# Kernel optimization log

Hardware: AMD Instinct MI355X
Metric: run time of the kernel (lower is better)

## Reference

```python
import jax, jax.numpy as jnp
import numpy as np

EPS = 1e-5
B, T, IN, EMD, CELL, OUT = 32768, 128, 2, 128, 128, 5


def batchnorm(x, gamma, beta):
    # BatchNorm1d in training mode: biased batch stats over batch dim
    mu = jnp.mean(x, axis=0, keepdims=True)
    var = jnp.var(x, axis=0, keepdims=True)
    return gamma * (x - mu) * jax.lax.rsqrt(var + EPS) + beta


def setup_inputs() -> dict:
    key = jax.random.key(0)
    ks = jax.random.split(key, 8)
    s = 0.05
    return {
        "inputs": jax.random.normal(ks[0], (B, T, IN), dtype=jnp.float32),
        # input embedding MLP: Linear(2,128) + BN + ReLU
        "w_emb": jax.random.normal(ks[1], (EMD, IN), dtype=jnp.float32) * s,
        "b_emb": jnp.zeros((EMD,), dtype=jnp.float32),
        "gamma1": jnp.ones((EMD,), dtype=jnp.float32),
        "beta1": jnp.zeros((EMD,), dtype=jnp.float32),
        # LSTMCell(emd_size, cell_size): gate order i,f,g,o
        "w_ih": jax.random.normal(ks[2], (4 * CELL, EMD), dtype=jnp.float32) * s,
        "w_hh": jax.random.normal(ks[3], (4 * CELL, CELL), dtype=jnp.float32) * s,
        "b_ih": jnp.zeros((4 * CELL,), dtype=jnp.float32),
        "b_hh": jnp.zeros((4 * CELL,), dtype=jnp.float32),
        # output MLP: Linear(128,5) + BN + ReLU
        "w_out": jax.random.normal(ks[4], (OUT, CELL), dtype=jnp.float32) * s,
        "b_out": jnp.zeros((OUT,), dtype=jnp.float32),
        "gamma2": jnp.ones((OUT,), dtype=jnp.float32),
        "beta2": jnp.zeros((OUT,), dtype=jnp.float32),
    }


def reference(inputs, w_emb, b_emb, gamma1, beta1, w_ih, w_hh, b_ih, b_hh,
              w_out, b_out, gamma2, beta2):
    x_tbd = jnp.transpose(inputs, (1, 0, 2))  # [T, B, IN]

    def step(carry, x_t):
        h, c = carry
        # input embedding MLP (train-mode BN + ReLU)
        e = jax.nn.relu(batchnorm(x_t @ w_emb.T + b_emb, gamma1, beta1))
        # LSTM cell
        gates = e @ w_ih.T + b_ih + h @ w_hh.T + b_hh  # [B, 4*CELL]
        i, f, g, o = jnp.split(gates, 4, axis=-1)
        c_new = jax.nn.sigmoid(f) * c + jax.nn.sigmoid(i) * jnp.tanh(g)
        h_new = jax.nn.sigmoid(o) * jnp.tanh(c_new)
        # output MLP (train-mode BN + ReLU)
        y = jax.nn.relu(batchnorm(h_new @ w_out.T + b_out, gamma2, beta2))
        return (h_new, c_new), y

    h0 = jnp.zeros((inputs.shape[0], CELL), dtype=inputs.dtype)
    c0 = jnp.zeros((inputs.shape[0], CELL), dtype=inputs.dtype)
    _, ys = jax.lax.scan(step, (h0, c0), x_tbd)  # ys: [T, B, OUT]
    return jnp.transpose(ys, (1, 0, 2))  # [B, T, OUT]
```

## Files before the change

### kernel.cpp

```cpp
#include <hip/hip_runtime.h>
#include <math.h>

#define B_    32768
#define T_    128
#define OUT_  5
#define EPS_  1e-5f

typedef float f32x4 __attribute__((ext_vector_type(4)));
typedef __bf16 bfrag __attribute__((ext_vector_type(8)));
typedef unsigned short ushort_t;

#define WS_WC2   0
#define WS_GB    67584
#define WS_A0    68112
#define WS_A1    84496
#define WS_C     100880
#define WS_IST   117264
#define WS_ZST   117904

__device__ __forceinline__ ushort_t f2bf(float f) {
  unsigned u = __float_as_uint(f);
  u += 0x7FFFu + ((u >> 16) & 1u);
  return (ushort_t)(u >> 16);
}
__device__ __forceinline__ float fsig(float x) {
  return __builtin_amdgcn_rcpf(1.f + __expf(-x));
}
__device__ __forceinline__ float ftanh(float x) {
  return 1.f - 2.f * __builtin_amdgcn_rcpf(1.f + __expf(2.f * x));
}

__global__ void k_istats(const float* __restrict__ x, float* __restrict__ istats) {
  const int tid = threadIdx.x;
  const int t = tid >> 1;
  const int i = tid & 1;
  const long b0 = (long)blockIdx.x * 64;
  float s_v = 0.f, s_vv = 0.f, s_cross = 0.f;
  for (int s = 0; s < 64; ++s) {
    float v = x[(b0 + s) * 256 + tid];
    float p = __shfl_xor(v, 1);
    s_v += v; s_vv += v * v; s_cross += v * p;
  }
  float* st = istats + t * 5;
  if (i == 0) {
    atomicAdd(st + 0, s_v); atomicAdd(st + 2, s_vv); atomicAdd(st + 4, s_cross);
  } else {
    atomicAdd(st + 1, s_v); atomicAdd(st + 3, s_vv);
  }
}

__global__ void k_prep_w(const float* __restrict__ w_ih, const float* __restrict__ w_hh,
                         const float* __restrict__ w_out, const float* __restrict__ b_ih,
                         const float* __restrict__ b_hh, const float* __restrict__ b_out,
                         ushort_t* __restrict__ Wc2, float* __restrict__ gbias) {
  int idx = blockIdx.x * 256 + threadIdx.x;
  int e = idx & 7;
  int lm = (idx >> 3) & 15;
  int lq = (idx >> 7) & 3;
  int ks = (idx >> 9) & 7;
  int T = idx >> 12;
  int k = ks * 32 + lq * 8 + e;
  float v;
  if (T < 32) {
    int g = T * 16 + lm;
    v = (k < 128) ? w_ih[g * 128 + k] : w_hh[g * 128 + (k - 128)];
  } else {
    v = (k >= 128 && lm < OUT_) ? w_out[lm * 128 + (k - 128)] : 0.f;
  }
  Wc2[idx] = f2bf(v);
  if (idx < 528) {
    float bv = (idx < 512) ? b_ih[idx] + b_hh[idx]
                           : (idx < 517 ? b_out[idx - 512] : 0.f);
    gbias[idx] = bv;
  }
}

__global__ void k_coef(const float* __restrict__ istats, const float* __restrict__ w_emb,
                       const float* __restrict__ b_emb, const float* __restrict__ gamma1,
                       const float* __restrict__ beta1, float* __restrict__ A0,
                       float* __restrict__ A1, float* __restrict__ C) {
  int idx = blockIdx.x * 256 + threadIdx.x;
  int t = idx >> 7, f = idx & 127;
  const float* st = istats + t * 5;
  const float invB = 1.f / (float)B_;
  float m0 = st[0] * invB, m1 = st[1] * invB;
  float v00 = st[2] * invB - m0 * m0;
  float v11 = st[3] * invB - m1 * m1;
  float c01 = st[4] * invB - m0 * m1;
  float w0 = w_emb[f * 2 + 0], w1 = w_emb[f * 2 + 1];
  float mu = m0 * w0 + m1 * w1 + b_emb[f];
  float var = w0 * w0 * v00 + w1 * w1 * v11 + 2.f * w0 * w1 * c01;
  float alpha = gamma1[f] * rsqrtf(var + EPS_);
  A0[t * 128 + f] = alpha * w0;
  A1[t * 128 + f] = alpha * w1;
  C[t * 128 + f] = alpha * (b_emb[f] - mu) + beta1[f];
}

__global__ __launch_bounds__(512, 2) void k_lstm(
    const float* __restrict__ x, const ushort_t* __restrict__ Wc2,
    const float* __restrict__ gbias, const float* __restrict__ A0,
    const float* __restrict__ A1, const float* __restrict__ Cc,
    float* __restrict__ out, float* __restrict__ zstats) {
  __shared__ __align__(16) ushort_t Abuf[128][520];
  __shared__ float zredS[2][8][5], zredQ[2][8][5];

  const int tid = threadIdx.x;
  const int w = tid >> 6;
  const int l = tid & 63;
  const int lm = l & 15;
  const int lq = l >> 4;
  const long b0 = (long)blockIdx.x * 128;

  const uint4* W4 = (const uint4*)Wc2;

  uint4 wreg[4][8];
#pragma unroll
  for (int i = 0; i < 4; ++i)
#pragma unroll
    for (int ks = 0; ks < 8; ++ks)
      wreg[i][ks] = W4[((w + 8 * i) * 8 + ks) * 64 + l];
  uint4 wzr[4];
#pragma unroll
  for (int i = 0; i < 4; ++i) wzr[i] = W4[(32 * 8 + 4 + i) * 64 + l];

  float bias_g[4];
#pragma unroll
  for (int i = 0; i < 4; ++i) bias_g[i] = gbias[(w + 8 * i) * 16 + lm];
  const float bias_z = gbias[512 + lm];

  const int em = (w << 4) + (l >> 2);
  const int ec = l & 3;
  const float2* x2 = (const float2*)x;

  float cst[8][4];
#pragma unroll
  for (int mt = 0; mt < 8; ++mt)
#pragma unroll
    for (int r = 0; r < 4; ++r) cst[mt][r] = 0.f;

  f32x4 zh0 = {0.f, 0.f, 0.f, 0.f}, zh1 = zh0, zh2 = zh0, zh3 = zh0;

  for (int i = tid; i < 128 * 520 / 8; i += 512)
    ((uint4*)&Abuf[0][0])[i] = make_uint4(0u, 0u, 0u, 0u);
  __syncthreads();

  for (int t = 0; t <= T_; ++t) {
    const int p = t & 1;
    const int pe = p * 128;
    const int ph = 256 + (p ^ 1) * 128;
    const int hw = 256 + p * 128;

    if (t < T_) {
      float2 xv = x2[(size_t)(b0 + em) * 128 + t];
#pragma unroll
      for (int pp = 0; pp < 4; ++pp) {
        const int f0 = pp * 32 + ec * 8;
        const f32x4 a0l = *(const f32x4*)(A0 + t * 128 + f0);
        const f32x4 a0h = *(const f32x4*)(A0 + t * 128 + f0 + 4);
        const f32x4 a1l = *(const f32x4*)(A1 + t * 128 + f0);
        const f32x4 a1h = *(const f32x4*)(A1 + t * 128 + f0 + 4);
        const f32x4 ccl = *(const f32x4*)(Cc + t * 128 + f0);
        const f32x4 cch = *(const f32x4*)(Cc + t * 128 + f0 + 4);
        unsigned pk[4];
#pragma unroll
        for (int h2 = 0; h2 < 4; ++h2) {
          float e0, e1;
          if (h2 < 2) {
            e0 = fmaf(xv.x, a0l[h2 * 2], fmaf(xv.y, a1l[h2 * 2], ccl[h2 * 2]));
            e1 = fmaf(xv.x, a0l[h2 * 2 + 1], fmaf(xv.y, a1l[h2 * 2 + 1], ccl[h2 * 2 + 1]));
          } else {
            e0 = fmaf(xv.x, a0h[(h2 - 2) * 2], fmaf(xv.y, a1h[(h2 - 2) * 2], cch[(h2 - 2) * 2]));
            e1 = fmaf(xv.x, a0h[(h2 - 2) * 2 + 1],
                      fmaf(xv.y, a1h[(h2 - 2) * 2 + 1], cch[(h2 - 2) * 2 + 1]));
          }
          e0 = fmaxf(e0, 0.f); e1 = fmaxf(e1, 0.f);
          pk[h2] = (unsigned)f2bf(e0) | ((unsigned)f2bf(e1) << 16);
        }
        *(uint4*)&Abuf[em][pe + f0] = make_uint4(pk[0], pk[1], pk[2], pk[3]);
      }
    }
    __syncthreads();

    if (t >= 2 && tid < 10) {
      const int o = tid >> 1, kind = tid & 1;
      float s = 0.f;
#pragma unroll
      for (int ww = 0; ww < 8; ++ww)
        s += kind ? zredQ[p ^ 1][ww][o] : zredS[p ^ 1][ww][o];
      atomicAdd(&zstats[(size_t)(t - 2) * 10 + o * 2 + kind], s);
    }

    const int colA = lq * 8;

#pragma unroll
    for (int mt = 0; mt < 8; ++mt) {
      const ushort_t* arow = &Abuf[mt * 16 + lm][0];
      f32x4 acc0 = {bias_g[0], bias_g[0], bias_g[0], bias_g[0]};
      f32x4 acc1 = {bias_g[1], bias_g[1], bias_g[1], bias_g[1]};
      f32x4 acc2 = {bias_g[2], bias_g[2], bias_g[2], bias_g[2]};
      f32x4 acc3 = {bias_g[3], bias_g[3], bias_g[3], bias_g[3]};
#pragma unroll
      for (int ks = 0; ks < 8; ++ks) {
        const int col = (ks < 4 ? pe + ks * 32 : ph + (ks - 4) * 32) + colA;
        const bfrag Af = __builtin_bit_cast(bfrag, *(const uint4*)(arow + col));
        acc0 = __builtin_amdgcn_mfma_f32_16x16x32_bf16(
            Af, __builtin_bit_cast(bfrag, wreg[0][ks]), acc0, 0, 0, 0);
        acc1 = __builtin_amdgcn_mfma_f32_16x16x32_bf16(
            Af, __builtin_bit_cast(bfrag, wreg[1][ks]), acc1, 0, 0, 0);
        acc2 = __builtin_amdgcn_mfma_f32_16x16x32_bf16(
            Af, __builtin_bit_cast(bfrag, wreg[2][ks]), acc2, 0, 0, 0);
        acc3 = __builtin_amdgcn_mfma_f32_16x16x32_bf16(
            Af, __builtin_bit_cast(bfrag, wreg[3][ks]), acc3, 0, 0, 0);
      }

      if (mt == w) {
        f32x4 zac = {bias_z, bias_z, bias_z, bias_z};
#pragma unroll
        for (int i = 0; i < 4; ++i) {
          const bfrag Af =
              __builtin_bit_cast(bfrag, *(const uint4*)(arow + ph + i * 32 + colA));
          zac = __builtin_amdgcn_mfma_f32_16x16x32_bf16(
              Af, __builtin_bit_cast(bfrag, wzr[i]), zac, 0, 0, 0);
        }
        if (t > 0) {
          float sz = 0.f, sq = 0.f;
#pragma unroll
          for (int r = 0; r < 4; ++r) {
            const float zv = zac[r];
            sz += zv; sq += zv * zv;
          }
          sz += __shfl_xor(sz, 16); sz += __shfl_xor(sz, 32);
          sq += __shfl_xor(sq, 16); sq += __shfl_xor(sq, 32);
          if (lq == 0 && lm < OUT_) { zredS[p][w][lm] = sz; zredQ[p][w][lm] = sq; }
          const int j = (t - 1) & 3;
          if (j == 0) zh0 = zac;
          else if (j == 1) zh1 = zac;
          else if (j == 2) zh2 = zac;
          else zh3 = zac;
          if (j == 3 && lm < OUT_) {
            const size_t sb0 = (size_t)(b0 + (w << 4) + lq * 4) * (T_ * OUT_) +
                               (size_t)(t - 4) * OUT_ + lm;
#pragma unroll
            for (int r = 0; r < 4; ++r) {
              const size_t sb = sb0 + (size_t)r * (T_ * OUT_);
              out[sb]            = zh0[r];
              out[sb + OUT_]     = zh1[r];
              out[sb + 2 * OUT_] = zh2[r];
              out[sb + 3 * OUT_] = zh3[r];
            }
          }
        }
      }

      if (t < T_) {
#pragma unroll
        for (int r = 0; r < 4; ++r) {
          const float gi = acc0[r], gf = acc1[r], gg = acc2[r], go = acc3[r];
          const float ig = fsig(gi), fg = fsig(gf), g2 = ftanh(gg), og = fsig(go);
          const float cn = fmaf(fg, cst[mt][r], ig * g2);
          cst[mt][r] = cn;
          const float h = og * ftanh(cn);
          Abuf[mt * 16 + lq * 4 + r][hw + (w << 4) + lm] = f2bf(h);
        }
      }
    }
  }

  __syncthreads();
  if (tid < 10) {
    const int o = tid >> 1, kind = tid & 1;
    float s = 0.f;
#pragma unroll
    for (int ww = 0; ww < 8; ++ww) s += kind ? zredQ[0][ww][o] : zredS[0][ww][o];
    atomicAdd(&zstats[(size_t)(T_ - 1) * 10 + o * 2 + kind], s);
  }
}

__global__ void k_outbn(float* __restrict__ out, const float* __restrict__ zstats,
                        const float* __restrict__ gamma2, const float* __restrict__ beta2) {
  int idx = blockIdx.x * 256 + threadIdx.x;
  int r = idx % 640;
  int t = r / 5, o = r - t * 5;
  float z = out[idx];
  float sum = zstats[t * 10 + o * 2];
  float ss = zstats[t * 10 + o * 2 + 1];
  float mu = sum * (1.f / (float)B_);
  float var = ss * (1.f / (float)B_) - mu * mu;
  float y = gamma2[o] * (z - mu) * rsqrtf(var + EPS_) + beta2[o];
  out[idx] = fmaxf(y, 0.f);
}

extern "C" void kernel_launch(void* const* d_in, const int* in_sizes, int n_in, void* d_out,
                              int out_size, void* d_ws, size_t ws_size, hipStream_t stream) {
  const float* x = (const float*)d_in[0];
  const float* w_emb = (const float*)d_in[1];
  const float* b_emb = (const float*)d_in[2];
  const float* gamma1 = (const float*)d_in[3];
  const float* beta1 = (const float*)d_in[4];
  const float* w_ih = (const float*)d_in[5];
  const float* w_hh = (const float*)d_in[6];
  const float* b_ih = (const float*)d_in[7];
  const float* b_hh = (const float*)d_in[8];
  const float* w_out = (const float*)d_in[9];
  const float* b_out = (const float*)d_in[10];
  const float* gamma2 = (const float*)d_in[11];
  const float* beta2 = (const float*)d_in[12];
  float* out = (float*)d_out;
  float* ws = (float*)d_ws;

  ushort_t* Wc2 = (ushort_t*)(ws + WS_WC2);
  float* gbias = ws + WS_GB;
  float* A0 = ws + WS_A0;
  float* A1 = ws + WS_A1;
  float* C = ws + WS_C;
  float* istats = ws + WS_IST;
  float* zstats = ws + WS_ZST;

  hipMemsetAsync(istats, 0, 640 * sizeof(float), stream);
  hipMemsetAsync(zstats, 0, 1280 * sizeof(float), stream);

  k_istats<<<512, 256, 0, stream>>>(x, istats);
  k_prep_w<<<528, 256, 0, stream>>>(w_ih, w_hh, w_out, b_ih, b_hh, b_out, Wc2, gbias);
  k_coef<<<64, 256, 0, stream>>>(istats, w_emb, b_emb, gamma1, beta1, A0, A1, C);
  k_lstm<<<256, 512, 0, stream>>>(x, Wc2, gbias, A0, A1, C, out, zstats);
  k_outbn<<<(B_ * T_ * OUT_) / 256, 256, 0, stream>>>(out, zstats, gamma2, beta2);
}
```

Measured before the change: 1.558 ms.

## Split LDS into swizzled E/H buffers and prefetch next-step embedding before barrier

Replaces the padded shared A buffer with separate double-buffered, XOR-swizzled embedding and hidden-state tiles. The next step's embedding is computed after the MFMA/gate work, so each timestep needs one barrier instead of two, and the extra t==T iteration becomes a peeled epilogue. It also switches to hardware bf16 pack conversion and raises wave priority around the MFMA block. This aims to cut barrier stalls, LDS bank conflicts and conversion ALU cost. The cost is more complex indexing and a separate tail path that must stay consistent with the per-step zstats/output handling.

```diff
diff --git a/kernel.cpp b/kernel.cpp
--- a/kernel.cpp
+++ b/kernel.cpp
@@ -22,6 +22,11 @@
   unsigned u = __float_as_uint(f);
   u += 0x7FFFu + ((u >> 16) & 1u);
   return (ushort_t)(u >> 16);
+}
+__device__ __forceinline__ unsigned cvtpk(float lo, float hi) {
+  unsigned r;
+  asm("v_cvt_pk_bf16_f32 %0, %1, %2" : "=v"(r) : "v"(lo), "v"(hi));
+  return r;
 }
 __device__ __forceinline__ float fsig(float x) {
   return __builtin_amdgcn_rcpf(1.f + __expf(-x));
@@ -96,12 +101,43 @@
   C[t * 128 + f] = alpha * (b_emb[f] - mu) + beta1[f];
 }
 
+__device__ __forceinline__ void stage_e(const float* __restrict__ A0,
+                                        const float* __restrict__ A1,
+                                        const float* __restrict__ Cc, int tt,
+                                        char* erow, float2 xv, const int* ewz, int ec) {
+  const float* A0t = A0 + tt * 128;
+  const float* A1t = A1 + tt * 128;
+  const float* Cct = Cc + tt * 128;
+#pragma unroll
+  for (int pp = 0; pp < 4; ++pp) {
+    const int f0 = pp * 32 + ec * 8;
+    const f32x4 a0l = *(const f32x4*)(A0t + f0);
+    const f32x4 a0h = *(const f32x4*)(A0t + f0 + 4);
+    const f32x4 a1l = *(const f32x4*)(A1t + f0);
+    const f32x4 a1h = *(const f32x4*)(A1t + f0 + 4);
+    const f32x4 ccl = *(const f32x4*)(Cct + f0);
+    const f32x4 cch = *(const f32x4*)(Cct + f0 + 4);
+    unsigned pk[4];
+#pragma unroll
+    for (int j = 0; j < 2; ++j) {
+      float e0 = fmaf(xv.x, a0l[2 * j],     fmaf(xv.y, a1l[2 * j],     ccl[2 * j]));
+      float e1 = fmaf(xv.x, a0l[2 * j + 1], fmaf(xv.y, a1l[2 * j + 1], ccl[2 * j + 1]));
+      pk[j] = cvtpk(fmaxf(e0, 0.f), fmaxf(e1, 0.f));
+      float e2 = fmaf(xv.x, a0h[2 * j],     fmaf(xv.y, a1h[2 * j],     cch[2 * j]));
+      float e3 = fmaf(xv.x, a0h[2 * j + 1], fmaf(xv.y, a1h[2 * j + 1], cch[2 * j + 1]));
+      pk[2 + j] = cvtpk(fmaxf(e2, 0.f), fmaxf(e3, 0.f));
+    }
+    *(uint4*)(erow + ewz[pp]) = make_uint4(pk[0], pk[1], pk[2], pk[3]);
+  }
+}
+
 __global__ __launch_bounds__(512, 2) void k_lstm(
     const float* __restrict__ x, const ushort_t* __restrict__ Wc2,
     const float* __restrict__ gbias, const float* __restrict__ A0,
     const float* __restrict__ A1, const float* __restrict__ Cc,
     float* __restrict__ out, float* __restrict__ zstats) {
-  __shared__ __align__(16) ushort_t Abuf[128][520];
+  __shared__ __align__(16) ushort_t Els[2][128][128];
+  __shared__ __align__(16) ushort_t Hls[2][128][128];
   __shared__ float zredS[2][8][5], zredQ[2][8][5];
 
   const int tid = threadIdx.x;
@@ -132,6 +168,16 @@
   const int ec = l & 3;
   const float2* x2 = (const float2*)x;
 
+  const int rowb = lm * 256;
+  int cswz[4], ewz[4], hoff[4];
+#pragma unroll
+  for (int i = 0; i < 4; ++i) {
+    cswz[i] = (((i * 4 + lq) ^ (lm & 7)) << 4);
+    ewz[i] = (((i * 4 + ec) ^ (em & 7)) << 4);
+    const int rr = lq * 4 + i;
+    hoff[i] = rr * 256 + ((((2 * w) + (lm >> 3)) ^ (rr & 7)) << 4) + ((lm & 7) << 1);
+  }
+
   float cst[8][4];
 #pragma unroll
   for (int mt = 0; mt < 8; ++mt)
@@ -140,46 +186,19 @@
 
   f32x4 zh0 = {0.f, 0.f, 0.f, 0.f}, zh1 = zh0, zh2 = zh0, zh3 = zh0;
 
-  for (int i = tid; i < 128 * 520 / 8; i += 512)
-    ((uint4*)&Abuf[0][0])[i] = make_uint4(0u, 0u, 0u, 0u);
+  for (int i = tid; i < 2048; i += 512)
+    ((uint4*)&Hls[1][0][0])[i] = make_uint4(0u, 0u, 0u, 0u);
+  {
+    float2 xv0 = x2[(size_t)(b0 + em) * 128 + 0];
+    stage_e(A0, A1, Cc, 0, (char*)&Els[0][0][0] + em * 256, xv0, ewz, ec);
+  }
   __syncthreads();
 
-  for (int t = 0; t <= T_; ++t) {
+  for (int t = 0; t < T_; ++t) {
     const int p = t & 1;
-    const int pe = p * 128;
-    const int ph = 256 + (p ^ 1) * 128;
-    const int hw = 256 + p * 128;
-
-    if (t < T_) {
-      float2 xv = x2[(size_t)(b0 + em) * 128 + t];
-#pragma unroll
-      for (int pp = 0; pp < 4; ++pp) {
-        const int f0 = pp * 32 + ec * 8;
-        const f32x4 a0l = *(const f32x4*)(A0 + t * 128 + f0);
-        const f32x4 a0h = *(const f32x4*)(A0 + t * 128 + f0 + 4);
-        const f32x4 a1l = *(const f32x4*)(A1 + t * 128 + f0);
-        const f32x4 a1h = *(const f32x4*)(A1 + t * 128 + f0 + 4);
-        const f32x4 ccl = *(const f32x4*)(Cc + t * 128 + f0);
-        const f32x4 cch = *(const f32x4*)(Cc + t * 128 + f0 + 4);
-        unsigned pk[4];
-#pragma unroll
-        for (int h2 = 0; h2 < 4; ++h2) {
-          float e0, e1;
-          if (h2 < 2) {
-            e0 = fmaf(xv.x, a0l[h2 * 2], fmaf(xv.y, a1l[h2 * 2], ccl[h2 * 2]));
-            e1 = fmaf(xv.x, a0l[h2 * 2 + 1], fmaf(xv.y, a1l[h2 * 2 + 1], ccl[h2 * 2 + 1]));
-          } else {
-            e0 = fmaf(xv.x, a0h[(h2 - 2) * 2], fmaf(xv.y, a1h[(h2 - 2) * 2], cch[(h2 - 2) * 2]));
-            e1 = fmaf(xv.x, a0h[(h2 - 2) * 2 + 1],
-                      fmaf(xv.y, a1h[(h2 - 2) * 2 + 1], cch[(h2 - 2) * 2 + 1]));
-          }
-          e0 = fmaxf(e0, 0.f); e1 = fmaxf(e1, 0.f);
-          pk[h2] = (unsigned)f2bf(e0) | ((unsigned)f2bf(e1) << 16);
-        }
-        *(uint4*)&Abuf[em][pe + f0] = make_uint4(pk[0], pk[1], pk[2], pk[3]);
-      }
-    }
-    __syncthreads();
+
+    float2 xv_nxt = make_float2(0.f, 0.f);
+    if (t + 1 < T_) xv_nxt = x2[(size_t)(b0 + em) * 128 + t + 1];
 
     if (t >= 2 && tid < 10) {
       const int o = tid >> 1, kind = tid & 1;
@@ -190,19 +209,23 @@
       atomicAdd(&zstats[(size_t)(t - 2) * 10 + o * 2 + kind], s);
     }
 
-    const int colA = lq * 8;
+    const char* Ep = (const char*)&Els[p][0][0];
+    const char* Hp1 = (const char*)&Hls[p ^ 1][0][0];
+    char* Hw = (char*)&Hls[p][0][0];
 
 #pragma unroll
     for (int mt = 0; mt < 8; ++mt) {
-      const ushort_t* arow = &Abuf[mt * 16 + lm][0];
+      const int mtoff = mt << 12;
+      const char* eb = Ep + mtoff + rowb;
+      const char* hb = Hp1 + mtoff + rowb;
       f32x4 acc0 = {bias_g[0], bias_g[0], bias_g[0], bias_g[0]};
       f32x4 acc1 = {bias_g[1], bias_g[1], bias_g[1], bias_g[1]};
       f32x4 acc2 = {bias_g[2], bias_g[2], bias_g[2], bias_g[2]};
       f32x4 acc3 = {bias_g[3], bias_g[3], bias_g[3], bias_g[3]};
-#pragma unroll
-      for (int ks = 0; ks < 8; ++ks) {
-        const int col = (ks < 4 ? pe + ks * 32 : ph + (ks - 4) * 32) + colA;
-        const bfrag Af = __builtin_bit_cast(bfrag, *(const uint4*)(arow + col));
+      __builtin_amdgcn_s_setprio(1);
+#pragma unroll
+      for (int ks = 0; ks < 4; ++ks) {
+        const bfrag Af = __builtin_bit_cast(bfrag, *(const uint4*)(eb + cswz[ks]));
         acc0 = __builtin_amdgcn_mfma_f32_16x16x32_bf16(
             Af, __builtin_bit_cast(bfrag, wreg[0][ks]), acc0, 0, 0, 0);
         acc1 = __builtin_amdgcn_mfma_f32_16x16x32_bf16(
@@ -212,47 +235,58 @@
         acc3 = __builtin_amdgcn_mfma_f32_16x16x32_bf16(
             Af, __builtin_bit_cast(bfrag, wreg[3][ks]), acc3, 0, 0, 0);
       }
-
-      if (mt == w) {
+#pragma unroll
+      for (int ks = 0; ks < 4; ++ks) {
+        const bfrag Af = __builtin_bit_cast(bfrag, *(const uint4*)(hb + cswz[ks]));
+        acc0 = __builtin_amdgcn_mfma_f32_16x16x32_bf16(
+            Af, __builtin_bit_cast(bfrag, wreg[0][4 + ks]), acc0, 0, 0, 0);
+        acc1 = __builtin_amdgcn_mfma_f32_16x16x32_bf16(
+            Af, __builtin_bit_cast(bfrag, wreg[1][4 + ks]), acc1, 0, 0, 0);
+        acc2 = __builtin_amdgcn_mfma_f32_16x16x32_bf16(
+            Af, __builtin_bit_cast(bfrag, wreg[2][4 + ks]), acc2, 0, 0, 0);
+        acc3 = __builtin_amdgcn_mfma_f32_16x16x32_bf16(
+            Af, __builtin_bit_cast(bfrag, wreg[3][4 + ks]), acc3, 0, 0, 0);
+      }
+      __builtin_amdgcn_s_setprio(0);
+
+      if (mt == w && t > 0) {
         f32x4 zac = {bias_z, bias_z, bias_z, bias_z};
 #pragma unroll
         for (int i = 0; i < 4; ++i) {
-          const bfrag Af =
-              __builtin_bit_cast(bfrag, *(const uint4*)(arow + ph + i * 32 + colA));
+          const bfrag Af = __builtin_bit_cast(bfrag, *(const uint4*)(hb + cswz[i]));
           zac = __builtin_amdgcn_mfma_f32_16x16x32_bf16(
               Af, __builtin_bit_cast(bfrag, wzr[i]), zac, 0, 0, 0);
         }
-        if (t > 0) {
-          float sz = 0.f, sq = 0.f;
+        float sz = 0.f, sq = 0.f;
+#pragma unroll
+        for (int r = 0; r < 4; ++r) {
+          const float zv = zac[r];
+          sz += zv; sq += zv * zv;
+        }
+        sz += __shfl_xor(sz, 16); sz += __shfl_xor(sz, 32);
+        sq += __shfl_xor(sq, 16); sq += __shfl_xor(sq, 32);
+        if (lq == 0 && lm < OUT_) { zredS[p][w][lm] = sz; zredQ[p][w][lm] = sq; }
+        const int j = (t - 1) & 3;
+        if (j == 0) zh0 = zac;
+        else if (j == 1) zh1 = zac;
+        else if (j == 2) zh2 = zac;
+        else zh3 = zac;
+        if (j == 3 && lm < OUT_) {
+          const size_t sb0 = (size_t)(b0 + (w << 4) + lq * 4) * (T_ * OUT_) +
+                             (size_t)(t - 4) * OUT_ + lm;
 #pragma unroll
           for (int r = 0; r < 4; ++r) {
-            const float zv = zac[r];
-            sz += zv; sq += zv * zv;
-          }
-          sz += __shfl_xor(sz, 16); sz += __shfl_xor(sz, 32);
-          sq += __shfl_xor(sq, 16); sq += __shfl_xor(sq, 32);
-          if (lq == 0 && lm < OUT_) { zredS[p][w][lm] = sz; zredQ[p][w][lm] = sq; }
-          const int j = (t - 1) & 3;
-          if (j == 0) zh0 = zac;
-          else if (j == 1) zh1 = zac;
-          else if (j == 2) zh2 = zac;
-          else zh3 = zac;
-          if (j == 3 && lm < OUT_) {
-            const size_t sb0 = (size_t)(b0 + (w << 4) + lq * 4) * (T_ * OUT_) +
-                               (size_t)(t - 4) * OUT_ + lm;
-#pragma unroll
-            for (int r = 0; r < 4; ++r) {
-              const size_t sb = sb0 + (size_t)r * (T_ * OUT_);
-              out[sb]            = zh0[r];
-              out[sb + OUT_]     = zh1[r];
-              out[sb + 2 * OUT_] = zh2[r];
-              out[sb + 3 * OUT_] = zh3[r];
-            }
+            const size_t sb = sb0 + (size_t)r * (T_ * OUT_);
+            out[sb]            = zh0[r];
+            out[sb + OUT_]     = zh1[r];
+            out[sb + 2 * OUT_] = zh2[r];
+            out[sb + 3 * OUT_] = zh3[r];
           }
         }
       }
 
-      if (t < T_) {
+      {
+        char* hwm = Hw + mtoff;
 #pragma unroll
         for (int r = 0; r < 4; ++r) {
           const float gi = acc0[r], gf = acc1[r], gg = acc2[r], go = acc3[r];
@@ -260,12 +294,56 @@
           const float cn = fmaf(fg, cst[mt][r], ig * g2);
           cst[mt][r] = cn;
           const float h = og * ftanh(cn);
-          Abuf[mt * 16 + lq * 4 + r][hw + (w << 4) + lm] = f2bf(h);
+          *(ushort_t*)(hwm + hoff[r]) = (ushort_t)cvtpk(h, h);
         }
       }
     }
-  }
-
+
+    if (t + 1 < T_)
+      stage_e(A0, A1, Cc, t + 1, (char*)&Els[p ^ 1][0][0] + em * 256, xv_nxt, ewz, ec);
+
+    __syncthreads();
+  }
+
+  if (tid < 10) {
+    const int o = tid >> 1, kind = tid & 1;
+    float s = 0.f;
+#pragma unroll
+    for (int ww = 0; ww < 8; ++ww) s += kind ? zredQ[1][ww][o] : zredS[1][ww][o];
+    atomicAdd(&zstats[(size_t)(T_ - 2) * 10 + o * 2 + kind], s);
+  }
+  {
+    const char* hb = (const char*)&Hls[1][0][0] + (w << 12) + rowb;
+    f32x4 zac = {bias_z, bias_z, bias_z, bias_z};
+#pragma unroll
+    for (int i = 0; i < 4; ++i) {
+      const bfrag Af = __builtin_bit_cast(bfrag, *(const uint4*)(hb + cswz[i]));
+      zac = __builtin_amdgcn_mfma_f32_16x16x32_bf16(
+          Af, __builtin_bit_cast(bfrag, wzr[i]), zac, 0, 0, 0);
+    }
+    float sz = 0.f, sq = 0.f;
+#pragma unroll
+    for (int r = 0; r < 4; ++r) {
+      const float zv = zac[r];
+      sz += zv; sq += zv * zv;
+    }
+    sz += __shfl_xor(sz, 16); sz += __shfl_xor(sz, 32);
+    sq += __shfl_xor(sq, 16); sq += __shfl_xor(sq, 32);
+    if (lq == 0 && lm < OUT_) { zredS[0][w][lm] = sz; zredQ[0][w][lm] = sq; }
+    zh3 = zac;
+    if (lm < OUT_) {
+      const size_t sb0 = (size_t)(b0 + (w << 4) + lq * 4) * (T_ * OUT_) +
+                         (size_t)(T_ - 4) * OUT_ + lm;
+#pragma unroll
+      for (int r = 0; r < 4; ++r) {
+        const size_t sb = sb0 + (size_t)r * (T_ * OUT_);
+        out[sb]            = zh0[r];
+        out[sb + OUT_]     = zh1[r];
+        out[sb + 2 * OUT_] = zh2[r];
+        out[sb + 3 * OUT_] = zh3[r];
+      }
+    }
+  }
   __syncthreads();
   if (tid < 10) {
     const int o = tid >> 1, kind = tid & 1;
```

Result: slower. 1.847 ms (+18.5%).

## Software-pipeline gate MFMAs with elementwise LSTM math and use hardware bf16 packing

Applied to the files above, without the earlier changes.

Restructures the per-timestep tile loop so the MFMA gate computation for tile mt is issued before the sigmoid/tanh/cell update of tile mt-1, using double-buffered accumulators. The aim is to overlap matrix-core work with VALU transcendental work. It also replaces the software round-to-nearest bf16 conversion with the v_cvt_pk_bf16_f32 instruction, and shortens the output staging from four timesteps to two. The extra live accumulators raise register pressure under launch_bounds(512,2), which risks spills.

```diff
diff --git a/kernel.cpp b/kernel.cpp
--- a/kernel.cpp
+++ b/kernel.cpp
@@ -22,6 +22,11 @@
   unsigned u = __float_as_uint(f);
   u += 0x7FFFu + ((u >> 16) & 1u);
   return (ushort_t)(u >> 16);
+}
+__device__ __forceinline__ unsigned cvtpk(float lo, float hi) {
+  unsigned r;
+  asm("v_cvt_pk_bf16_f32 %0, %1, %2" : "=v"(r) : "v"(lo), "v"(hi));
+  return r;
 }
 __device__ __forceinline__ float fsig(float x) {
   return __builtin_amdgcn_rcpf(1.f + __expf(-x));
@@ -96,6 +101,81 @@
   C[t * 128 + f] = alpha * (b_emb[f] - mu) + beta1[f];
 }
 
+#define GATE_TILE(MT, PB)                                                         \
+  {                                                                               \
+    const ushort_t* arow_ = &Abuf[(MT) * 16 + lm][0];                             \
+    _Pragma("unroll")                                                             \
+    for (int i = 0; i < 4; ++i) {                                                 \
+      f32x4 v_ = {bias_g[i], bias_g[i], bias_g[i], bias_g[i]};                    \
+      acc[PB][i] = v_;                                                            \
+    }                                                                             \
+    _Pragma("unroll")                                                             \
+    for (int ks = 0; ks < 8; ++ks) {                                              \
+      const int col_ = (ks < 4 ? pe + ks * 32 : ph + (ks - 4) * 32) + lq * 8;     \
+      const bfrag Af_ = __builtin_bit_cast(bfrag, *(const uint4*)(arow_ + col_)); \
+      _Pragma("unroll")                                                           \
+      for (int i = 0; i < 4; ++i)                                                 \
+        acc[PB][i] = __builtin_amdgcn_mfma_f32_16x16x32_bf16(                     \
+            Af_, __builtin_bit_cast(bfrag, wreg[i][ks]), acc[PB][i], 0, 0, 0);    \
+    }                                                                             \
+    if ((MT) == w && t > 0) {                                                     \
+      const ushort_t* hrow_ = &Abuf[w * 16 + lm][0];                              \
+      f32x4 z_ = {bias_z, bias_z, bias_z, bias_z};                                \
+      _Pragma("unroll")                                                           \
+      for (int i = 0; i < 4; ++i) {                                               \
+        const bfrag Ah_ = __builtin_bit_cast(                                     \
+            bfrag, *(const uint4*)(hrow_ + ph + i * 32 + lq * 8));                \
+        z_ = __builtin_amdgcn_mfma_f32_16x16x32_bf16(                             \
+            Ah_, __builtin_bit_cast(bfrag, wzr[i]), z_, 0, 0, 0);                 \
+      }                                                                           \
+      zac = z_;                                                                   \
+    }                                                                             \
+  }
+
+#define EW_TILE(MT, PB)                                                           \
+  {                                                                               \
+    if ((MT) == w && t > 0) {                                                     \
+      float sz_ = 0.f, sq_ = 0.f;                                                 \
+      _Pragma("unroll")                                                           \
+      for (int r = 0; r < 4; ++r) {                                               \
+        const float zv_ = zac[r];                                                 \
+        sz_ += zv_; sq_ += zv_ * zv_;                                             \
+      }                                                                           \
+      sz_ += __shfl_xor(sz_, 16); sz_ += __shfl_xor(sz_, 32);                     \
+      sq_ += __shfl_xor(sq_, 16); sq_ += __shfl_xor(sq_, 32);                     \
+      if (lq == 0 && lm < OUT_) { zredS[p][w][lm] = sz_; zredQ[p][w][lm] = sq_; } \
+      if (((t - 1) & 1) == 0) {                                                   \
+        zh0 = zac;                                                                \
+      } else {                                                                    \
+        zh1 = zac;                                                                \
+        if (lm < OUT_) {                                                          \
+          const size_t sb0_ = (size_t)(b0 + (w << 4) + lq * 4) * (T_ * OUT_) +    \
+                              (size_t)(t - 2) * OUT_ + lm;                        \
+          _Pragma("unroll")                                                       \
+          for (int r = 0; r < 4; ++r) {                                           \
+            const size_t sb_ = sb0_ + (size_t)r * (T_ * OUT_);                    \
+            out[sb_] = zh0[r];                                                    \
+            out[sb_ + OUT_] = zh1[r];                                             \
+          }                                                                       \
+        }                                                                         \
+      }                                                                           \
+    }                                                                             \
+    if (t < T_) {                                                                 \
+      _Pragma("unroll")                                                           \
+      for (int r = 0; r < 4; ++r) {                                               \
+        const float gi_ = acc[PB][0][r], gf_ = acc[PB][1][r];                     \
+        const float gg_ = acc[PB][2][r], go_ = acc[PB][3][r];                     \
+        const float ig_ = fsig(gi_), fg_ = fsig(gf_);                             \
+        const float g2_ = ftanh(gg_), og_ = fsig(go_);                            \
+        const float cn_ = fmaf(fg_, cst[MT][r], ig_ * g2_);                       \
+        cst[MT][r] = cn_;                                                         \
+        const float h_ = og_ * ftanh(cn_);                                        \
+        Abuf[(MT) * 16 + lq * 4 + r][hw + (w << 4) + lm] =                        \
+            (ushort_t)cvtpk(h_, h_);                                              \
+      }                                                                           \
+    }                                                                             \
+  }
+
 __global__ __launch_bounds__(512, 2) void k_lstm(
     const float* __restrict__ x, const ushort_t* __restrict__ Wc2,
     const float* __restrict__ gbias, const float* __restrict__ A0,
@@ -138,7 +218,7 @@
 #pragma unroll
     for (int r = 0; r < 4; ++r) cst[mt][r] = 0.f;
 
-  f32x4 zh0 = {0.f, 0.f, 0.f, 0.f}, zh1 = zh0, zh2 = zh0, zh3 = zh0;
+  f32x4 zh0 = {0.f, 0.f, 0.f, 0.f}, zh1 = zh0;
 
   for (int i = tid; i < 128 * 520 / 8; i += 512)
     ((uint4*)&Abuf[0][0])[i] = make_uint4(0u, 0u, 0u, 0u);
@@ -152,29 +232,27 @@
 
     if (t < T_) {
       float2 xv = x2[(size_t)(b0 + em) * 128 + t];
+      const float* A0t = A0 + t * 128;
+      const float* A1t = A1 + t * 128;
+      const float* Cct = Cc + t * 128;
 #pragma unroll
       for (int pp = 0; pp < 4; ++pp) {
         const int f0 = pp * 32 + ec * 8;
-        const f32x4 a0l = *(const f32x4*)(A0 + t * 128 + f0);
-        const f32x4 a0h = *(const f32x4*)(A0 + t * 128 + f0 + 4);
-        const f32x4 a1l = *(const f32x4*)(A1 + t * 128 + f0);
-        const f32x4 a1h = *(const f32x4*)(A1 + t * 128 + f0 + 4);
-        const f32x4 ccl = *(const f32x4*)(Cc + t * 128 + f0);
-        const f32x4 cch = *(const f32x4*)(Cc + t * 128 + f0 + 4);
+        const f32x4 a0l = *(const f32x4*)(A0t + f0);
+        const f32x4 a0h = *(const f32x4*)(A0t + f0 + 4);
+        const f32x4 a1l = *(const f32x4*)(A1t + f0);
+        const f32x4 a1h = *(const f32x4*)(A1t + f0 + 4);
+        const f32x4 ccl = *(const f32x4*)(Cct + f0);
+        const f32x4 cch = *(const f32x4*)(Cct + f0 + 4);
         unsigned pk[4];
 #pragma unroll
-        for (int h2 = 0; h2 < 4; ++h2) {
-          float e0, e1;
-          if (h2 < 2) {
-            e0 = fmaf(xv.x, a0l[h2 * 2], fmaf(xv.y, a1l[h2 * 2], ccl[h2 * 2]));
-            e1 = fmaf(xv.x, a0l[h2 * 2 + 1], fmaf(xv.y, a1l[h2 * 2 + 1], ccl[h2 * 2 + 1]));
-          } else {
-            e0 = fmaf(xv.x, a0h[(h2 - 2) * 2], fmaf(xv.y, a1h[(h2 - 2) * 2], cch[(h2 - 2) * 2]));
-            e1 = fmaf(xv.x, a0h[(h2 - 2) * 2 + 1],
-                      fmaf(xv.y, a1h[(h2 - 2) * 2 + 1], cch[(h2 - 2) * 2 + 1]));
-          }
-          e0 = fmaxf(e0, 0.f); e1 = fmaxf(e1, 0.f);
-          pk[h2] = (unsigned)f2bf(e0) | ((unsigned)f2bf(e1) << 16);
+        for (int j = 0; j < 2; ++j) {
+          float e0 = fmaf(xv.x, a0l[2 * j],     fmaf(xv.y, a1l[2 * j],     ccl[2 * j]));
+          float e1 = fmaf(xv.x, a0l[2 * j + 1], fmaf(xv.y, a1l[2 * j + 1], ccl[2 * j + 1]));
+          pk[j] = cvtpk(fmaxf(e0, 0.f), fmaxf(e1, 0.f));
+          float e2 = fmaf(xv.x, a0h[2 * j],     fmaf(xv.y, a1h[2 * j],     cch[2 * j]));
+          float e3 = fmaf(xv.x, a0h[2 * j + 1], fmaf(xv.y, a1h[2 * j + 1], cch[2 * j + 1]));
+          pk[2 + j] = cvtpk(fmaxf(e2, 0.f), fmaxf(e3, 0.f));
         }
         *(uint4*)&Abuf[em][pe + f0] = make_uint4(pk[0], pk[1], pk[2], pk[3]);
       }
@@ -190,80 +268,15 @@
       atomicAdd(&zstats[(size_t)(t - 2) * 10 + o * 2 + kind], s);
     }
 
-    const int colA = lq * 8;
-
-#pragma unroll
-    for (int mt = 0; mt < 8; ++mt) {
-      const ushort_t* arow = &Abuf[mt * 16 + lm][0];
-      f32x4 acc0 = {bias_g[0], bias_g[0], bias_g[0], bias_g[0]};
-      f32x4 acc1 = {bias_g[1], bias_g[1], bias_g[1], bias_g[1]};
-      f32x4 acc2 = {bias_g[2], bias_g[2], bias_g[2], bias_g[2]};
-      f32x4 acc3 = {bias_g[3], bias_g[3], bias_g[3], bias_g[3]};
-#pragma unroll
-      for (int ks = 0; ks < 8; ++ks) {
-        const int col = (ks < 4 ? pe + ks * 32 : ph + (ks - 4) * 32) + colA;
-        const bfrag Af = __builtin_bit_cast(bfrag, *(const uint4*)(arow + col));
-        acc0 = __builtin_amdgcn_mfma_f32_16x16x32_bf16(
-            Af, __builtin_bit_cast(bfrag, wreg[0][ks]), acc0, 0, 0, 0);
-        acc1 = __builtin_amdgcn_mfma_f32_16x16x32_bf16(
-            Af, __builtin_bit_cast(bfrag, wreg[1][ks]), acc1, 0, 0, 0);
-        acc2 = __builtin_amdgcn_mfma_f32_16x16x32_bf16(
-            Af, __builtin_bit_cast(bfrag, wreg[2][ks]), acc2, 0, 0, 0);
-        acc3 = __builtin_amdgcn_mfma_f32_16x16x32_bf16(
-            Af, __builtin_bit_cast(bfrag, wreg[3][ks]), acc3, 0, 0, 0);
-      }
-
-      if (mt == w) {
-        f32x4 zac = {bias_z, bias_z, bias_z, bias_z};
-#pragma unroll
-        for (int i = 0; i < 4; ++i) {
-          const bfrag Af =
-              __builtin_bit_cast(bfrag, *(const uint4*)(arow + ph + i * 32 + colA));
-          zac = __builtin_amdgcn_mfma_f32_16x16x32_bf16(
-              Af, __builtin_bit_cast(bfrag, wzr[i]), zac, 0, 0, 0);
-        }
-        if (t > 0) {
-          float sz = 0.f, sq = 0.f;
-#pragma unroll
-          for (int r = 0; r < 4; ++r) {
-            const float zv = zac[r];
-            sz += zv; sq += zv * zv;
-          }
-          sz += __shfl_xor(sz, 16); sz += __shfl_xor(sz, 32);
-          sq += __shfl_xor(sq, 16); sq += __shfl_xor(sq, 32);
-          if (lq == 0 && lm < OUT_) { zredS[p][w][lm] = sz; zredQ[p][w][lm] = sq; }
-          const int j = (t - 1) & 3;
-          if (j == 0) zh0 = zac;
-          else if (j == 1) zh1 = zac;
-          else if (j == 2) zh2 = zac;
-          else zh3 = zac;
-          if (j == 3 && lm < OUT_) {
-            const size_t sb0 = (size_t)(b0 + (w << 4) + lq * 4) * (T_ * OUT_) +
-                               (size_t)(t - 4) * OUT_ + lm;
-#pragma unroll
-            for (int r = 0; r < 4; ++r) {
-              const size_t sb = sb0 + (size_t)r * (T_ * OUT_);
-              out[sb]            = zh0[r];
-              out[sb + OUT_]     = zh1[r];
-              out[sb + 2 * OUT_] = zh2[r];
-              out[sb + 3 * OUT_] = zh3[r];
-            }
-          }
-        }
-      }
-
-      if (t < T_) {
-#pragma unroll
-        for (int r = 0; r < 4; ++r) {
-          const float gi = acc0[r], gf = acc1[r], gg = acc2[r], go = acc3[r];
-          const float ig = fsig(gi), fg = fsig(gf), g2 = ftanh(gg), og = fsig(go);
-          const float cn = fmaf(fg, cst[mt][r], ig * g2);
-          cst[mt][r] = cn;
-          const float h = og * ftanh(cn);
-          Abuf[mt * 16 + lq * 4 + r][hw + (w << 4) + lm] = f2bf(h);
-        }
-      }
+    f32x4 acc[2][4];
+    f32x4 zac = {0.f, 0.f, 0.f, 0.f};
+    GATE_TILE(0, 0)
+#pragma unroll
+    for (int mt = 1; mt < 8; ++mt) {
+      GATE_TILE(mt, (mt & 1))
+      EW_TILE((mt - 1), ((mt - 1) & 1))
     }
+    EW_TILE(7, 1)
   }
 
   __syncthreads();
```

Result: faster. 1.524 ms (-2.2%).
